# Performance work log

Hardware: AMD Instinct MI355X
Metric: run time of the kernel (lower is better)

## Reference

```python
import jax, jax.numpy as jnp
import numpy as np

EMBED = 1024  # point_net_embedding_dim
H1, H2 = 512, 256  # head_hidden_layer_sizes


def _init(key, shape, fan_in):
    return jax.random.normal(key, shape, dtype=jnp.float32) / jnp.sqrt(jnp.float32(fan_in))


def setup_inputs() -> dict:
    key = jax.random.key(0)
    ks = jax.random.split(key, 13)
    B, N = 256, 1024
    x = jax.random.normal(ks[0], (B, N, 3), dtype=jnp.float32)
    # PointNet shared per-point MLP: 3 -> 64 -> 128 -> EMBED (ReLU), max-pool over points
    W1 = _init(ks[1], (3, 64), 3);        b1 = jnp.zeros((64,), jnp.float32)
    W2 = _init(ks[2], (64, 128), 64);     b2 = jnp.zeros((128,), jnp.float32)
    W3 = _init(ks[3], (128, EMBED), 128); b3 = jnp.zeros((EMBED,), jnp.float32)
    # Head MLP: EMBED -> 512 -> 256 -> 9 (no final activation)
    Wh1 = _init(ks[4], (EMBED, H1), EMBED); bh1 = jnp.zeros((H1,), jnp.float32)
    Wh2 = _init(ks[5], (H1, H2), H1);       bh2 = jnp.zeros((H2,), jnp.float32)
    Wh3 = _init(ks[6], (H2, 9), H2);        bh3 = jnp.zeros((9,), jnp.float32)
    return {"x": x, "W1": W1, "b1": b1, "W2": W2, "b2": b2, "W3": W3, "b3": b3,
            "Wh1": Wh1, "bh1": bh1, "Wh2": Wh2, "bh2": bh2, "Wh3": Wh3, "bh3": bh3}


def svd_projection(M):
    # Project raw 3x3 matrices onto SO(3): R = U diag(1,1,det(U V^T)) V^T
    U, S, Vh = jnp.linalg.svd(M, full_matrices=False)
    det = jnp.linalg.det(jnp.einsum('...ij,...jk->...ik', U, Vh))
    d = jnp.stack([jnp.ones_like(det), jnp.ones_like(det), det], axis=-1)  # [..., 3]
    return jnp.einsum('...ij,...j,...jk->...ik', U, d, Vh)


def reference(x, W1, b1, W2, b2, W3, b3, Wh1, bh1, Wh2, bh2, Wh3, bh3):
    # Shared per-point MLP (ReLU), final_activation=ReLU, then max-pool over points
    h = jax.nn.relu(x @ W1 + b1)          # [B, N, 64]
    h = jax.nn.relu(h @ W2 + b2)          # [B, N, 128]
    h = jax.nn.relu(h @ W3 + b3)          # [B, N, EMBED]
    g = jnp.max(h, axis=-2)               # [B, EMBED] global feature
    # Head MLP -> raw 3x3
    z = jax.nn.relu(g @ Wh1 + bh1)
    z = jax.nn.relu(z @ Wh2 + bh2)
    raw = (z @ Wh3 + bh3).reshape(*x.shape[:-2], 3, 3)
    return svd_projection(raw)
```

## Files before the change

### kernel.cpp

```cpp
#include <hip/hip_runtime.h>
#include <math.h>

typedef _Float16 f16;
typedef _Float16 f16x8 __attribute__((ext_vector_type(8)));
typedef float f32x4 __attribute__((ext_vector_type(4)));

__device__ __forceinline__ void glds16(const void* g, void* l) {
    __builtin_amdgcn_global_load_lds(
        (const __attribute__((address_space(1))) unsigned int*)g,
        (__attribute__((address_space(3))) unsigned int*)l, 16, 0, 0);
}

__global__ __launch_bounds__(256, 2) void pointnet_l12(
    const float* __restrict__ x,
    const float* __restrict__ W1, const float* __restrict__ b1,
    const float* __restrict__ W2, const float* __restrict__ b2,
    f16* __restrict__ h2)
{
    __shared__ float xs[512*3];
    __shared__ float w1s[192], b1s[64], b2s[128];
    __shared__ __align__(16) f16 h2s[128*136];

    int tid = threadIdx.x;
    int P0 = blockIdx.x * 512;
    for (int i = tid; i < 1536; i += 256) xs[i] = x[(size_t)P0*3 + i];
    if (tid < 192) w1s[tid] = W1[tid];
    else b1s[tid - 192] = b1[tid - 192];
    if (tid < 128) b2s[tid] = b2[tid];

    int lane = tid & 63, wid = tid >> 6;
    int wr = wid & 1, wc = wid >> 1;
    int lrow = lane & 15, quad = lane >> 4;

    f16x8 bf[4][2];
#pragma unroll
    for (int ct = 0; ct < 4; ct++)
#pragma unroll
        for (int kc = 0; kc < 2; kc++) {
            int col = wc*64 + ct*16 + lrow;
#pragma unroll
            for (int j = 0; j < 8; j++)
                bf[ct][kc][j] = (f16)W2[(size_t)(kc*32 + quad*8 + j)*128 + col];
        }

    __syncthreads();

    for (int mt = 0; mt < 4; mt++) {
        f32x4 acc[4][4];
#pragma unroll
        for (int rt = 0; rt < 4; rt++)
#pragma unroll
            for (int ct = 0; ct < 4; ct++)
                acc[rt][ct] = (f32x4){0.f, 0.f, 0.f, 0.f};

#pragma unroll
        for (int kc = 0; kc < 2; kc++) {
            float wa[8], wb[8], wcv[8], bv[8];
#pragma unroll
            for (int j = 0; j < 8; j++) {
                int k = kc*32 + quad*8 + j;
                wa[j] = w1s[k]; wb[j] = w1s[64+k]; wcv[j] = w1s[128+k]; bv[j] = b1s[k];
            }
            f16x8 af[4];
#pragma unroll
            for (int rt = 0; rt < 4; rt++) {
                int p = mt*128 + wr*64 + rt*16 + lrow;
                float x0 = xs[p*3], x1 = xs[p*3+1], x2 = xs[p*3+2];
#pragma unroll
                for (int j = 0; j < 8; j++) {
                    float v = fmaf(x2, wcv[j], fmaf(x1, wb[j], fmaf(x0, wa[j], bv[j])));
                    af[rt][j] = (f16)fmaxf(v, 0.f);
                }
            }
#pragma unroll
            for (int rt = 0; rt < 4; rt++)
#pragma unroll
                for (int ct = 0; ct < 4; ct++)
                    acc[rt][ct] = __builtin_amdgcn_mfma_f32_16x16x32_f16(af[rt], bf[ct][kc], acc[rt][ct], 0, 0, 0);
        }

        __syncthreads();
#pragma unroll
        for (int rt = 0; rt < 4; rt++)
#pragma unroll
            for (int ct = 0; ct < 4; ct++) {
                int col  = wc*64 + ct*16 + lrow;
                float bb = b2s[col];
                int rowb = wr*64 + rt*16 + quad*4;
#pragma unroll
                for (int r = 0; r < 4; r++) {
                    float v = fmaxf(acc[rt][ct][r] + bb, 0.f);
                    h2s[(rowb + r)*136 + col] = (f16)v;
                }
            }
        __syncthreads();
        size_t gbase = ((size_t)P0 + (size_t)mt*128) * 128;
#pragma unroll
        for (int i = 0; i < 8; i++) {
            int e = i*256 + tid;
            int row = e >> 4, c = e & 15;
            f16x8 v = *(const f16x8*)(h2s + row*136 + c*8);
            *(f16x8*)(h2 + gbase + (size_t)row*128 + ((c ^ (row & 15)) * 8)) = v;
        }
    }
}

__global__ __launch_bounds__(256, 2) void pointnet_l3_max(
    const f16* __restrict__ h2,
    const float* __restrict__ W3,
    const float* __restrict__ b3,
    float* __restrict__ g)
{
    __shared__ __align__(16) f16 atile[2][128 * 128];

    int i  = blockIdx.x;
    int b  = i & 255, nb = i >> 8;
    int tid = threadIdx.x;
    int lane = tid & 63, wid = tid >> 6;
    int lrow = lane & 15, quad = lane >> 4;
    int col0 = nb*256 + wid*64;

    f16x8 bf[4][4];
#pragma unroll
    for (int ct = 0; ct < 4; ct++)
#pragma unroll
        for (int kc = 0; kc < 4; kc++) {
            int col = col0 + ct*16 + lrow;
#pragma unroll
            for (int j = 0; j < 8; j++)
                bf[ct][kc][j] = (f16)W3[(size_t)(kc*32 + quad*8 + j)*1024 + col];
        }

    float cmax[4] = {-3.0e38f, -3.0e38f, -3.0e38f, -3.0e38f};
    const f16* abase = h2 + (size_t)b * 1024 * 128;

    {
        const f16* gsrc = abase;
#pragma unroll
        for (int s = 0; s < 8; s++)
            glds16(gsrc + (wid*512 + s*64 + lane)*8, atile[0] + (wid*512 + s*64)*8);
    }

    int cur = 0;
    for (int m0 = 0; m0 < 1024; m0 += 128) {
        __syncthreads();
        if (m0 + 128 < 1024) {
            const f16* gsrc = abase + (size_t)(m0 + 128) * 128;
            f16* ldst = atile[cur ^ 1];
#pragma unroll
            for (int s = 0; s < 8; s++)
                glds16(gsrc + (wid*512 + s*64 + lane)*8, ldst + (wid*512 + s*64)*8);
        }

        const f16* at = atile[cur];
#pragma unroll
        for (int half = 0; half < 2; half++) {
            f32x4 acc[4][4];
#pragma unroll
            for (int rt = 0; rt < 4; rt++)
#pragma unroll
                for (int ct = 0; ct < 4; ct++)
                    acc[rt][ct] = (f32x4){0.f, 0.f, 0.f, 0.f};
#pragma unroll
            for (int kc = 0; kc < 4; kc++) {
                f16x8 af[4];
#pragma unroll
                for (int rt = 0; rt < 4; rt++) {
                    int row  = half*64 + rt*16 + lrow;
                    int slot = (kc*4 + quad) ^ lrow;
                    af[rt] = *(const f16x8*)(at + row*128 + slot*8);
                }
#pragma unroll
                for (int rt = 0; rt < 4; rt++)
#pragma unroll
                    for (int ct = 0; ct < 4; ct++)
                        acc[rt][ct] = __builtin_amdgcn_mfma_f32_16x16x32_f16(af[rt], bf[ct][kc], acc[rt][ct], 0, 0, 0);
            }
#pragma unroll
            for (int rt = 0; rt < 4; rt++)
#pragma unroll
                for (int ct = 0; ct < 4; ct++)
#pragma unroll
                    for (int r = 0; r < 4; r++)
                        cmax[ct] = fmaxf(cmax[ct], acc[rt][ct][r]);
        }
        cur ^= 1;
    }

#pragma unroll
    for (int ct = 0; ct < 4; ct++) {
        cmax[ct] = fmaxf(cmax[ct], __shfl_xor(cmax[ct], 16, 64));
        cmax[ct] = fmaxf(cmax[ct], __shfl_xor(cmax[ct], 32, 64));
    }
    if (quad == 0) {
#pragma unroll
        for (int ct = 0; ct < 4; ct++) {
            int cg = col0 + ct*16 + lrow;
            g[(size_t)b*1024 + cg] = fmaxf(cmax[ct] + b3[cg], 0.f);
        }
    }
}

__global__ __launch_bounds__(256) void head_l1(
    const float* __restrict__ g, const float* __restrict__ Wh1,
    float* __restrict__ zp1)
{
    __shared__ float gs4[4][256];
    int cb = blockIdx.x, bb = blockIdx.y, kc = blockIdx.z;
    int tid = threadIdx.x;
    int b0 = bb * 4;
    int kbase = kc * 256;
#pragma unroll
    for (int j = 0; j < 4; j++) {
        int i = tid + j*256;
        gs4[i >> 8][i & 255] = g[(size_t)(b0 + (i >> 8))*1024 + kbase + (i & 255)];
    }
    __syncthreads();

    int c = cb*256 + tid;
    float acc[4] = {0.f, 0.f, 0.f, 0.f};
#pragma unroll 1
    for (int k = 0; k < 256; k += 8) {
        float w[8];
#pragma unroll
        for (int j = 0; j < 8; j++) w[j] = Wh1[(size_t)(kbase+k+j)*512 + c];
#pragma unroll
        for (int r = 0; r < 4; r++) {
            float4 a = *(const float4*)&gs4[r][k];
            float4 bq = *(const float4*)&gs4[r][k+4];
            acc[r] = fmaf(a.x, w[0], acc[r]);
            acc[r] = fmaf(a.y, w[1], acc[r]);
            acc[r] = fmaf(a.z, w[2], acc[r]);
            acc[r] = fmaf(a.w, w[3], acc[r]);
            acc[r] = fmaf(bq.x, w[4], acc[r]);
            acc[r] = fmaf(bq.y, w[5], acc[r]);
            acc[r] = fmaf(bq.z, w[6], acc[r]);
            acc[r] = fmaf(bq.w, w[7], acc[r]);
        }
    }
#pragma unroll
    for (int r = 0; r < 4; r++)
        zp1[((size_t)kc*256 + b0 + r)*512 + c] = acc[r];
}

__global__ __launch_bounds__(256) void head_l2(
    const float* __restrict__ zp1, const float* __restrict__ bh1,
    const float* __restrict__ Wh2, float* __restrict__ zp2)
{
    __shared__ float z1s[2][128];
    int bb = blockIdx.x, kc2 = blockIdx.y;
    int tid = threadIdx.x;
    int b0 = bb * 2;
    int kb = kc2 * 128;
    {
        int row = tid >> 7, kk = tid & 127;
        int col = kb + kk;
        float v = bh1[col];
#pragma unroll
        for (int j = 0; j < 4; j++)
            v += zp1[((size_t)j*256 + b0 + row)*512 + col];
        z1s[row][kk] = fmaxf(v, 0.f);
    }
    __syncthreads();

    int c = tid;
    float acc0 = 0.f, acc1 = 0.f;
#pragma unroll 1
    for (int k = 0; k < 128; k += 8) {
        float w[8];
#pragma unroll
        for (int j = 0; j < 8; j++) w[j] = Wh2[(size_t)(kb+k+j)*256 + c];
        float4 a0 = *(const float4*)&z1s[0][k];
        float4 a1 = *(const float4*)&z1s[0][k+4];
        float4 d0 = *(const float4*)&z1s[1][k];
        float4 d1 = *(const float4*)&z1s[1][k+4];
        acc0 = fmaf(a0.x, w[0], acc0);  acc1 = fmaf(d0.x, w[0], acc1);
        acc0 = fmaf(a0.y, w[1], acc0);  acc1 = fmaf(d0.y, w[1], acc1);
        acc0 = fmaf(a0.z, w[2], acc0);  acc1 = fmaf(d0.z, w[2], acc1);
        acc0 = fmaf(a0.w, w[3], acc0);  acc1 = fmaf(d0.w, w[3], acc1);
        acc0 = fmaf(a1.x, w[4], acc0);  acc1 = fmaf(d1.x, w[4], acc1);
        acc0 = fmaf(a1.y, w[5], acc0);  acc1 = fmaf(d1.y, w[5], acc1);
        acc0 = fmaf(a1.z, w[6], acc0);  acc1 = fmaf(d1.z, w[6], acc1);
        acc0 = fmaf(a1.w, w[7], acc0);  acc1 = fmaf(d1.w, w[7], acc1);
    }
    zp2[((size_t)kc2*256 + b0    )*256 + c] = acc0;
    zp2[((size_t)kc2*256 + b0 + 1)*256 + c] = acc1;
}

__device__ inline void jrot(double S[3][3], double V[3][3], int p, int q)
{
    double apq = S[p][q];
    if (fabs(apq) < 1e-36) return;
    double tau = (S[q][q] - S[p][p]) / (2.0 * apq);
    double t = (tau >= 0.0 ? 1.0 : -1.0) / (fabs(tau) + sqrt(1.0 + tau*tau));
    double c = 1.0 / sqrt(1.0 + t*t);
    double s = t * c;
    for (int k = 0; k < 3; k++) {
        double skp = S[k][p], skq = S[k][q];
        S[k][p] = c*skp - s*skq;  S[k][q] = s*skp + c*skq;
    }
    for (int k = 0; k < 3; k++) {
        double spk = S[p][k], sqk = S[q][k];
        S[p][k] = c*spk - s*sqk;  S[q][k] = s*spk + c*sqk;
    }
    for (int k = 0; k < 3; k++) {
        double vkp = V[k][p], vkq = V[k][q];
        V[k][p] = c*vkp - s*vkq;  V[k][q] = s*vkp + c*vkq;
    }
}

__device__ void svd_so3(const float* Mf, float* Rout)
{
    double M[3][3], S[3][3], V[3][3];
    for (int i = 0; i < 3; i++)
        for (int j = 0; j < 3; j++) M[i][j] = (double)Mf[3*i+j];
    for (int i = 0; i < 3; i++)
        for (int j = 0; j < 3; j++)
            S[i][j] = M[0][i]*M[0][j] + M[1][i]*M[1][j] + M[2][i]*M[2][j];
    for (int i = 0; i < 3; i++)
        for (int j = 0; j < 3; j++) V[i][j] = (i == j) ? 1.0 : 0.0;
    for (int it = 0; it < 10; it++) {
        jrot(S, V, 0, 1); jrot(S, V, 0, 2); jrot(S, V, 1, 2);
    }
    double lam[3] = {S[0][0], S[1][1], S[2][2]};
    int i0 = 0, i1 = 1, i2 = 2, tt;
    if (lam[i0] < lam[i1]) { tt = i0; i0 = i1; i1 = tt; }
    if (lam[i0] < lam[i2]) { tt = i0; i0 = i2; i2 = tt; }
    if (lam[i1] < lam[i2]) { tt = i1; i1 = i2; i2 = tt; }
    double v0[3], v1[3], v2[3];
    for (int k = 0; k < 3; k++) { v0[k] = V[k][i0]; v1[k] = V[k][i1]; v2[k] = V[k][i2]; }
    double u1[3], u2[3], u3[3];
    for (int i = 0; i < 3; i++) u1[i] = M[i][0]*v0[0] + M[i][1]*v0[1] + M[i][2]*v0[2];
    double n1 = sqrt(u1[0]*u1[0] + u1[1]*u1[1] + u1[2]*u1[2]) + 1e-300;
    for (int i = 0; i < 3; i++) u1[i] /= n1;
    for (int i = 0; i < 3; i++) u2[i] = M[i][0]*v1[0] + M[i][1]*v1[1] + M[i][2]*v1[2];
    double d12 = u1[0]*u2[0] + u1[1]*u2[1] + u1[2]*u2[2];
    for (int i = 0; i < 3; i++) u2[i] -= d12*u1[i];
    double n2 = sqrt(u2[0]*u2[0] + u2[1]*u2[1] + u2[2]*u2[2]) + 1e-300;
    for (int i = 0; i < 3; i++) u2[i] /= n2;
    u3[0] = u1[1]*u2[2] - u1[2]*u2[1];
    u3[1] = u1[2]*u2[0] - u1[0]*u2[2];
    u3[2] = u1[0]*u2[1] - u1[1]*u2[0];
    double c12x = v1[1]*v2[2] - v1[2]*v2[1];
    double c12y = v1[2]*v2[0] - v1[0]*v2[2];
    double c12z = v1[0]*v2[1] - v1[1]*v2[0];
    double detV = v0[0]*c12x + v0[1]*c12y + v0[2]*c12z;
    for (int i = 0; i < 3; i++)
        for (int j = 0; j < 3; j++)
            Rout[3*i+j] = (float)(u1[i]*v0[j] + u2[i]*v1[j] + detV*u3[i]*v2[j]);
}

__global__ __launch_bounds__(128) void head_l3_svd(
    const float* __restrict__ zp2, const float* __restrict__ bh2,
    const float* __restrict__ Wh3, const float* __restrict__ bh3,
    float* __restrict__ out)
{
    __shared__ float z2s[8][256];
    __shared__ float wh3s[2304];
    __shared__ float raws[8][12];
    int b0 = blockIdx.x * 8;
    int tid = threadIdx.x;

    for (int i = tid; i < 2304; i += 128) wh3s[i] = Wh3[i];
    for (int i = tid; i < 8*256; i += 128) {
        int row = i >> 8, kk = i & 255;
        float v = bh2[kk];
#pragma unroll
        for (int j = 0; j < 4; j++)
            v += zp2[((size_t)j*256 + b0 + row)*256 + kk];
        z2s[row][kk] = fmaxf(v, 0.f);
    }
    __syncthreads();

    if (tid < 72) {
        int r = tid / 9, c = tid % 9;
        float acc = bh3[c];
#pragma unroll 8
        for (int k = 0; k < 256; k++) acc = fmaf(z2s[r][k], wh3s[k*9 + c], acc);
        raws[r][c] = acc;
    }
    __syncthreads();

    if (tid < 8) svd_so3(&raws[tid][0], out + (size_t)(b0 + tid)*9);
}

extern "C" void kernel_launch(void* const* d_in, const int* in_sizes, int n_in,
                              void* d_out, int out_size, void* d_ws, size_t ws_size,
                              hipStream_t stream)
{
    const float* x   = (const float*)d_in[0];
    const float* W1  = (const float*)d_in[1];
    const float* b1  = (const float*)d_in[2];
    const float* W2  = (const float*)d_in[3];
    const float* b2  = (const float*)d_in[4];
    const float* W3  = (const float*)d_in[5];
    const float* b3  = (const float*)d_in[6];
    const float* Wh1 = (const float*)d_in[7];
    const float* bh1 = (const float*)d_in[8];
    const float* Wh2 = (const float*)d_in[9];
    const float* bh2 = (const float*)d_in[10];
    const float* Wh3 = (const float*)d_in[11];
    const float* bh3 = (const float*)d_in[12];
    float* out = (float*)d_out;

    char* ws = (char*)d_ws;
    f16*   h2  = (f16*)ws;
    float* g   = (float*)(ws + (size_t)67108864);
    float* zp1 = (float*)(ws + (size_t)67108864 + 1048576);
    float* zp2 = (float*)(ws + (size_t)67108864 + 1048576 + 2097152);

    pointnet_l12<<<512, 256, 0, stream>>>(x, W1, b1, W2, b2, h2);
    pointnet_l3_max<<<1024, 256, 0, stream>>>(h2, W3, b3, g);
    dim3 gridH1(2, 64, 4);
    head_l1<<<gridH1, 256, 0, stream>>>(g, Wh1, zp1);
    dim3 gridH2(128, 4);
    head_l2<<<gridH2, 256, 0, stream>>>(zp1, bh1, Wh2, zp2);
    head_l3_svd<<<32, 128, 0, stream>>>(zp2, bh2, Wh3, bh3, out);
}
```

Before: 189.4 us.

## Read layer-3 A fragments directly from global instead of LDS double-buffering

Drops the LDS double-buffered tile staging (global_load_lds plus barriers) in the layer-3 max kernel and has each lane load its MFMA A fragments straight from global memory, relying on cache reuse across the column-block workgroups. Because the LDS swizzle is no longer needed, the producer kernel now writes h2 unswizzled. Without the LDS footprint, launch bounds are raised to allow 3 blocks per SM, and the max reduction is restructured into pairwise fmax. The risk is higher global/L2 traffic and exposed load latency with no explicit prefetch.

```diff
diff --git a/kernel.cpp b/kernel.cpp
--- a/kernel.cpp
+++ b/kernel.cpp
@@ -4,12 +4,6 @@
 typedef _Float16 f16;
 typedef _Float16 f16x8 __attribute__((ext_vector_type(8)));
 typedef float f32x4 __attribute__((ext_vector_type(4)));
-
-__device__ __forceinline__ void glds16(const void* g, void* l) {
-    __builtin_amdgcn_global_load_lds(
-        (const __attribute__((address_space(1))) unsigned int*)g,
-        (__attribute__((address_space(3))) unsigned int*)l, 16, 0, 0);
-}
 
 __global__ __launch_bounds__(256, 2) void pointnet_l12(
     const float* __restrict__ x,
@@ -100,19 +94,17 @@
             int e = i*256 + tid;
             int row = e >> 4, c = e & 15;
             f16x8 v = *(const f16x8*)(h2s + row*136 + c*8);
-            *(f16x8*)(h2 + gbase + (size_t)row*128 + ((c ^ (row & 15)) * 8)) = v;
-        }
-    }
-}
-
-__global__ __launch_bounds__(256, 2) void pointnet_l3_max(
+            *(f16x8*)(h2 + gbase + (size_t)row*128 + c*8) = v;
+        }
+    }
+}
+
+__global__ __launch_bounds__(256, 3) void pointnet_l3_max(
     const f16* __restrict__ h2,
     const float* __restrict__ W3,
     const float* __restrict__ b3,
     float* __restrict__ g)
 {
-    __shared__ __align__(16) f16 atile[2][128 * 128];
-
     int i  = blockIdx.x;
     int b  = i & 255, nb = i >> 8;
     int tid = threadIdx.x;
@@ -132,27 +124,9 @@
         }
 
     float cmax[4] = {-3.0e38f, -3.0e38f, -3.0e38f, -3.0e38f};
-    const f16* abase = h2 + (size_t)b * 1024 * 128;
-
-    {
-        const f16* gsrc = abase;
-#pragma unroll
-        for (int s = 0; s < 8; s++)
-            glds16(gsrc + (wid*512 + s*64 + lane)*8, atile[0] + (wid*512 + s*64)*8);
-    }
-
-    int cur = 0;
+    const f16* abase = h2 + (size_t)b * 1024 * 128 + (size_t)lrow * 128 + quad * 8;
+
     for (int m0 = 0; m0 < 1024; m0 += 128) {
-        __syncthreads();
-        if (m0 + 128 < 1024) {
-            const f16* gsrc = abase + (size_t)(m0 + 128) * 128;
-            f16* ldst = atile[cur ^ 1];
-#pragma unroll
-            for (int s = 0; s < 8; s++)
-                glds16(gsrc + (wid*512 + s*64 + lane)*8, ldst + (wid*512 + s*64)*8);
-        }
-
-        const f16* at = atile[cur];
 #pragma unroll
         for (int half = 0; half < 2; half++) {
             f32x4 acc[4][4];
@@ -165,11 +139,8 @@
             for (int kc = 0; kc < 4; kc++) {
                 f16x8 af[4];
 #pragma unroll
-                for (int rt = 0; rt < 4; rt++) {
-                    int row  = half*64 + rt*16 + lrow;
-                    int slot = (kc*4 + quad) ^ lrow;
-                    af[rt] = *(const f16x8*)(at + row*128 + slot*8);
-                }
+                for (int rt = 0; rt < 4; rt++)
+                    af[rt] = *(const f16x8*)(abase + (size_t)(m0 + half*64 + rt*16)*128 + kc*32);
 #pragma unroll
                 for (int rt = 0; rt < 4; rt++)
 #pragma unroll
@@ -181,10 +152,9 @@
 #pragma unroll
                 for (int ct = 0; ct < 4; ct++)
 #pragma unroll
-                    for (int r = 0; r < 4; r++)
-                        cmax[ct] = fmaxf(cmax[ct], acc[rt][ct][r]);
-        }
-        cur ^= 1;
+                    for (int r = 0; r < 4; r += 2)
+                        cmax[ct] = fmaxf(fmaxf(acc[rt][ct][r], acc[rt][ct][r+1]), cmax[ct]);
+        }
     }
 
 #pragma unroll
```

Measured after the change: 297.1 us. 56.9% more time.
